# Kernel optimization log

Measured on AMD Instinct MI355X. Metric: run time of the kernel, lower is better.

Reference implementation:

```python
import jax, jax.numpy as jnp
import numpy as np

N_NODES = 100000
N_EDGES = 1600000
N_FEAT = 128
HIDDEN = 128
OUT = 1
NUM_GRAPHS = 2048


def setup_inputs() -> dict:
    key = jax.random.key(0)
    ks = jax.random.split(key, 8)
    x = jax.random.normal(ks[0], (N_NODES, N_FEAT), dtype=jnp.float32)
    edge_index = jax.random.randint(ks[1], (2, N_EDGES), 0, N_NODES, dtype=jnp.int64)
    batch = jnp.sort(jax.random.randint(ks[2], (N_NODES,), 0, NUM_GRAPHS, dtype=jnp.int64))
    s = 1.0 / np.sqrt(N_FEAT)
    W1 = jax.random.normal(ks[3], (N_FEAT, HIDDEN), dtype=jnp.float32) * s
    b1 = jnp.zeros((HIDDEN,), dtype=jnp.float32)
    W2 = jax.random.normal(ks[4], (HIDDEN, HIDDEN), dtype=jnp.float32) * s
    b2 = jnp.zeros((HIDDEN,), dtype=jnp.float32)
    Wlin = jax.random.normal(ks[5], (HIDDEN, OUT), dtype=jnp.float32) * s
    blin = jnp.zeros((OUT,), dtype=jnp.float32)
    return {"x": x, "edge_index": edge_index, "batch": batch,
            "W1": W1, "b1": b1, "W2": W2, "b2": b2, "Wlin": Wlin, "blin": blin}


def gcn_conv(x, W, b, src, dst, n_nodes):
    # PyG GCNConv: x' = D^{-1/2} (A + I) D^{-1/2} (X W) + b, deg includes self-loop
    xw = x @ W  # [N, H]
    deg = jax.ops.segment_sum(jnp.ones(src.shape[0], xw.dtype), dst, num_segments=n_nodes) + 1.0
    dinv = jax.lax.rsqrt(deg)
    norm = dinv[src] * dinv[dst]  # [E]
    agg = jax.ops.segment_sum(xw[src] * norm[:, None], dst, num_segments=n_nodes)
    # self-loop contribution: norm = deg^{-1}
    return agg + xw * (1.0 / deg)[:, None] + b


def global_mean_pool(x, batch, num_graphs):
    sums = jax.ops.segment_sum(x, batch, num_segments=num_graphs)
    cnts = jax.ops.segment_sum(jnp.ones(x.shape[0], x.dtype), batch, num_segments=num_graphs)
    return sums / jnp.maximum(cnts, 1.0)[:, None]


def reference(x, edge_index, batch, W1, b1, W2, b2, Wlin, blin):
    src, dst = edge_index[0], edge_index[1]
    n = x.shape[0]
    h = gcn_conv(x, W1, b1, src, dst, n)
    h = jax.nn.relu(h)  # dropout is a no-op in eval mode
    h = gcn_conv(h, W2, b2, src, dst, n)
    g = global_mean_pool(h, batch, NUM_GRAPHS)  # [G, H]
    return g @ Wlin + blin
```

## Files before the change

kernel.cpp:

```cpp
#include <hip/hip_runtime.h>

#define N_NODES   100000
#define N_EDGES   1600000
#define NFEAT     128
#define NGRAPHS   2048
#define CBSHIFT   8
#define NCB       ((N_NODES + 255) / 256)
#define P1_EPB    8192
#define GEMM_BLOCKS 782
#define BH_BLOCKS   256
#define DP_BLOCKS 100
#define DP_NPB    ((N_NODES + DP_BLOCKS - 1) / DP_BLOCKS)
#define G1_BLOCKS 2048
#define ZCNT      (NGRAPHS + NCB + 64 + 512 + NCB)

typedef __attribute__((ext_vector_type(8))) short short8;
typedef __attribute__((ext_vector_type(4))) float f32x4;

__device__ __forceinline__ unsigned short f2bf(float f) {
    unsigned int u = __float_as_uint(f);
    u += 0x7FFFu + ((u >> 16) & 1u);
    return (unsigned short)(u >> 16);
}

__device__ __forceinline__ void acc8s(float* acc, uint4 v, float s) {
    acc[0] = fmaf(s, __uint_as_float(v.x << 16), acc[0]);
    acc[1] = fmaf(s, __uint_as_float(v.x & 0xFFFF0000u), acc[1]);
    acc[2] = fmaf(s, __uint_as_float(v.y << 16), acc[2]);
    acc[3] = fmaf(s, __uint_as_float(v.y & 0xFFFF0000u), acc[3]);
    acc[4] = fmaf(s, __uint_as_float(v.z << 16), acc[4]);
    acc[5] = fmaf(s, __uint_as_float(v.z & 0xFFFF0000u), acc[5]);
    acc[6] = fmaf(s, __uint_as_float(v.w << 16), acc[6]);
    acc[7] = fmaf(s, __uint_as_float(v.w & 0xFFFF0000u), acc[7]);
}

__global__ __launch_bounds__(256) void k_misc(const float* __restrict__ W1,
                                              unsigned short* __restrict__ WT1,
                                              const float* __restrict__ W2,
                                              const float* __restrict__ Wlin,
                                              const float* __restrict__ b2,
                                              const float* __restrict__ blin,
                                              float* __restrict__ w2l,
                                              int* __restrict__ zeros) {
    const int blk = blockIdx.x;
    const int t = threadIdx.x;
    if (blk < 16) {
        int base = blk * 1024 + t * 4;
        #pragma unroll
        for (int q = 0; q < 4; ++q) {
            int i = base + q;
            int n = i >> 7, k = i & 127;
            WT1[i] = f2bf(W1[k * 128 + n]);
        }
    } else if (blk == 16) {
        __shared__ float s[256];
        int i = t >> 1, half = t & 1;
        float ps = 0.f;
        for (int j = half * 64; j < half * 64 + 64; ++j)
            ps += W2[i * 128 + j] * Wlin[j];
        s[t] = ps;
        __syncthreads();
        if (!half) w2l[i] = s[t] + s[t + 1];
        __syncthreads();
        float pc = (t < 128) ? b2[t] * Wlin[t] : 0.f;
        s[t] = pc;
        __syncthreads();
        for (int off = 128; off > 0; off >>= 1) {
            if (t < off) s[t] += s[t + off];
            __syncthreads();
        }
        if (t == 0) w2l[128] = s[0] + blin[0];
    } else {
        int i = (blk - 17) * 256 + t;
        if (i < ZCNT) zeros[i] = 0;
    }
}

__global__ __launch_bounds__(256) void k_gemm_bhist(const float* __restrict__ X,
                                                    const unsigned short* __restrict__ WT,
                                                    unsigned short* __restrict__ C,
                                                    const int* __restrict__ dst,
                                                    int* __restrict__ bcount) {
    if (blockIdx.x >= GEMM_BLOCKS) {
        __shared__ int h[NCB];
        for (int i = threadIdx.x; i < NCB; i += 256) h[i] = 0;
        __syncthreads();
        int b = blockIdx.x - GEMM_BLOCKS;
        int stride = BH_BLOCKS * 256;
        for (int e = b * 256 + threadIdx.x; e < N_EDGES; e += stride)
            atomicAdd(&h[dst[e] >> CBSHIFT], 1);
        __syncthreads();
        for (int i = threadIdx.x; i < NCB; i += 256) {
            int v = h[i];
            if (v) atomicAdd(&bcount[i], v);
        }
        return;
    }
    const int tid  = threadIdx.x;
    const int R0   = blockIdx.x * 128;
    const int wv   = tid >> 6;
    const int lane = tid & 63;
    const int m16  = lane & 15;
    const int quad = lane >> 4;
    const int r0 = R0 + wv * 32 + m16;
    const int r1 = r0 + 16;
    const bool ok0 = r0 < N_NODES, ok1 = r1 < N_NODES;

    f32x4 acc[2][8] = {};
    #pragma unroll
    for (int ks = 0; ks < 4; ++ks) {
        const int k0 = ks * 32 + quad * 8;
        short8 a0 = {}, a1 = {};
        if (ok0) {
            float4 f0 = *(const float4*)(X + (size_t)r0 * NFEAT + k0);
            float4 f1 = *(const float4*)(X + (size_t)r0 * NFEAT + k0 + 4);
            a0[0] = (short)f2bf(f0.x); a0[1] = (short)f2bf(f0.y);
            a0[2] = (short)f2bf(f0.z); a0[3] = (short)f2bf(f0.w);
            a0[4] = (short)f2bf(f1.x); a0[5] = (short)f2bf(f1.y);
            a0[6] = (short)f2bf(f1.z); a0[7] = (short)f2bf(f1.w);
        }
        if (ok1) {
            float4 f0 = *(const float4*)(X + (size_t)r1 * NFEAT + k0);
            float4 f1 = *(const float4*)(X + (size_t)r1 * NFEAT + k0 + 4);
            a1[0] = (short)f2bf(f0.x); a1[1] = (short)f2bf(f0.y);
            a1[2] = (short)f2bf(f0.z); a1[3] = (short)f2bf(f0.w);
            a1[4] = (short)f2bf(f1.x); a1[5] = (short)f2bf(f1.y);
            a1[6] = (short)f2bf(f1.z); a1[7] = (short)f2bf(f1.w);
        }
        #pragma unroll
        for (int ct = 0; ct < 8; ++ct) {
            short8 bb = *(const short8*)(WT + (ct * 16 + m16) * 128 + k0);
            acc[0][ct] = __builtin_amdgcn_mfma_f32_16x16x32_bf16(a0, bb, acc[0][ct], 0, 0, 0);
            acc[1][ct] = __builtin_amdgcn_mfma_f32_16x16x32_bf16(a1, bb, acc[1][ct], 0, 0, 0);
        }
    }
    #pragma unroll
    for (int t2 = 0; t2 < 2; ++t2) {
        int rbase = R0 + wv * 32 + t2 * 16 + quad * 4;
        #pragma unroll
        for (int reg = 0; reg < 4; ++reg) {
            int gr = rbase + reg;
            if (gr < N_NODES) {
                #pragma unroll
                for (int ct = 0; ct < 8; ++ct)
                    C[(size_t)gr * NFEAT + ct * 16 + m16] = f2bf(acc[t2][ct][reg]);
            }
        }
    }
}

__global__ __launch_bounds__(256) void k_p1(const int* __restrict__ src,
                                            const int* __restrict__ dst,
                                            const int* __restrict__ bcount,
                                            int* __restrict__ bstart,
                                            int* __restrict__ alloc,
                                            unsigned int* __restrict__ pairs) {
    __shared__ int hist[NCB], base[NCB], cur[NCB], bst[NCB], s[256];
    const int t = threadIdx.x;
    for (int i = t; i < NCB; i += 256) { hist[i] = 0; cur[i] = 0; }
    int v0 = (2 * t < NCB) ? bcount[2 * t] : 0;
    int v1 = (2 * t + 1 < NCB) ? bcount[2 * t + 1] : 0;
    int local = v0 + v1;
    s[t] = local;
    __syncthreads();
    for (int off = 1; off < 256; off <<= 1) {
        int x = (t >= off) ? s[t - off] : 0;
        __syncthreads();
        s[t] += x;
        __syncthreads();
    }
    int excl = s[t] - local;
    if (2 * t < NCB)     bst[2 * t] = excl;
    if (2 * t + 1 < NCB) bst[2 * t + 1] = excl + v0;
    if (blockIdx.x == 0) {
        if (2 * t < NCB)     bstart[2 * t] = excl;
        if (2 * t + 1 < NCB) bstart[2 * t + 1] = excl + v0;
        if (t == 255) bstart[NCB] = s[255];
    }
    __syncthreads();
    const int e0 = blockIdx.x * P1_EPB;
    const int e1 = min(e0 + P1_EPB, N_EDGES);
    for (int e = e0 + t; e < e1; e += 256)
        atomicAdd(&hist[dst[e] >> CBSHIFT], 1);
    __syncthreads();
    const int off0 = (blockIdx.x * 89) % NCB;
    for (int k = t; k < NCB; k += 256) {
        int i = k + off0;
        if (i >= NCB) i -= NCB;
        int c = hist[i];
        base[i] = c ? (bst[i] + atomicAdd(&alloc[i], c)) : 0;
    }
    __syncthreads();
    for (int e = e0 + t; e < e1; e += 256) {
        int d = dst[e];
        int b = d >> CBSHIFT;
        int r = atomicAdd(&cur[b], 1);
        pairs[base[b] + r] = (unsigned int)src[e] | ((unsigned int)(d & 255) << 17);
    }
}

__global__ __launch_bounds__(256) void k_p2(const unsigned int* __restrict__ pairs,
                                            const int* __restrict__ bstart,
                                            int* __restrict__ csr_src,
                                            int* __restrict__ row_start,
                                            int* __restrict__ indeg,
                                            float* __restrict__ dinv,
                                            int* __restrict__ dcount) {
    __shared__ int hist[256], sst[256], cur[256], s[256], dh[64];
    const int b = blockIdx.x;
    const int t = threadIdx.x;
    const int beg = bstart[b];
    const int end = bstart[b + 1];
    hist[t] = 0; cur[t] = 0;
    if (t < 64) dh[t] = 0;
    __syncthreads();
    for (int i = beg + t; i < end; i += 256)
        atomicAdd(&hist[pairs[i] >> 17], 1);
    __syncthreads();
    int v = hist[t];
    s[t] = v;
    __syncthreads();
    for (int off = 1; off < 256; off <<= 1) {
        int x = (t >= off) ? s[t - off] : 0;
        __syncthreads();
        s[t] += x;
        __syncthreads();
    }
    sst[t] = s[t] - v;
    __syncthreads();
    {
        int node = (b << CBSHIFT) + t;
        if (node < N_NODES) {
            row_start[node] = beg + sst[t];
            indeg[node] = v;
            dinv[node] = rsqrtf((float)v + 1.0f);
            atomicAdd(&dh[63 - min(v, 63)], 1);
        }
    }
    for (int i = beg + t; i < end; i += 256) {
        unsigned int pv = pairs[i];
        int dl = pv >> 17;
        int r = atomicAdd(&cur[dl], 1);
        csr_src[beg + sst[dl] + r] = (int)(pv & 0x1FFFFu);
    }
    __syncthreads();
    if (t < 64 && dh[t]) atomicAdd(&dcount[((b & 7) << 6) + t], dh[t]);
}

__global__ __launch_bounds__(256) void k_dperm(const int* __restrict__ indeg,
                                               const int* __restrict__ dcount,
                                               int* __restrict__ dalloc,
                                               int* __restrict__ perm) {
    __shared__ int h[64], base[64], cur[64], s[64];
    const int t = threadIdx.x;
    int v = 0;
    if (t < 64) {
        h[t] = 0; cur[t] = 0;
        #pragma unroll
        for (int sh = 0; sh < 8; ++sh) v += dcount[(sh << 6) + t];
        s[t] = v;
    }
    __syncthreads();
    for (int off = 1; off < 64; off <<= 1) {
        int x = (t >= off && t < 64) ? s[t - off] : 0;
        __syncthreads();
        if (t < 64) s[t] += x;
        __syncthreads();
    }
    int myst = (t < 64) ? s[t] - v : 0;
    const int i0 = blockIdx.x * DP_NPB;
    const int i1 = min(i0 + DP_NPB, N_NODES);
    for (int i = i0 + t; i < i1; i += 256)
        atomicAdd(&h[63 - min(indeg[i], 63)], 1);
    __syncthreads();
    if (t < 64) {
        int c = h[t];
        base[t] = c ? (myst + atomicAdd(&dalloc[t], c)) : 0;
    }
    __syncthreads();
    for (int i = i0 + t; i < i1; i += 256) {
        int bin = 63 - min(indeg[i], 63);
        int r = atomicAdd(&cur[bin], 1);
        perm[base[bin] + r] = i;
    }
}

__global__ __launch_bounds__(256) void k_gather1(const unsigned short* __restrict__ xwb,
                                                 const int* __restrict__ csr_src,
                                                 const int* __restrict__ row_start,
                                                 const int* __restrict__ indeg,
                                                 const float* __restrict__ dinv,
                                                 const float* __restrict__ b,
                                                 const float* __restrict__ w2l,
                                                 const int* __restrict__ perm,
                                                 float* __restrict__ z) {
    const int lane  = threadIdx.x & 63;
    const int p     = lane & 15;
    const int gbase = lane & 48;
    const int ngroups = G1_BLOCKS * 16;
    int gid = blockIdx.x * 16 + (threadIdx.x >> 4);
    const uint4* tab = (const uint4*)xwb;
    float4 b0 = *(const float4*)(b + p * 8);
    float4 b1 = *(const float4*)(b + p * 8 + 4);
    float4 w0 = *(const float4*)(w2l + p * 8);
    float4 w1 = *(const float4*)(w2l + p * 8 + 4);

    for (int nidx = gid; nidx < N_NODES; nidx += ngroups) {
        int node = perm[nidx];
        const int beg = row_start[node];
        const int cnt = indeg[node];
        float dvn = dinv[node];
        float acc[8] = {};
        acc8s(acc, tab[(size_t)node * 16 + p], dvn);
        int j = 0;
        #pragma unroll 1
        for (; j + 8 <= cnt; j += 8) {
            int   my   = csr_src[beg + j + (p & 7)];
            float mydv = dinv[my];
            uint4 v[8];
            #pragma unroll
            for (int q = 0; q < 8; ++q) {
                int idx = __shfl(my, gbase + q);
                v[q] = tab[(size_t)idx * 16 + p];
            }
            #pragma unroll
            for (int q = 0; q < 8; ++q) {
                float sv = __shfl(mydv, gbase + q);
                acc8s(acc, v[q], sv);
            }
        }
        #pragma unroll 1
        for (; j < cnt; ++j) {
            int idx = csr_src[beg + j];
            float sv = dinv[idx];
            acc8s(acc, tab[(size_t)idx * 16 + p], sv);
        }
        float s = fmaxf(acc[0] * dvn + b0.x, 0.f) * w0.x
                + fmaxf(acc[1] * dvn + b0.y, 0.f) * w0.y
                + fmaxf(acc[2] * dvn + b0.z, 0.f) * w0.z
                + fmaxf(acc[3] * dvn + b0.w, 0.f) * w0.w
                + fmaxf(acc[4] * dvn + b1.x, 0.f) * w1.x
                + fmaxf(acc[5] * dvn + b1.y, 0.f) * w1.y
                + fmaxf(acc[6] * dvn + b1.z, 0.f) * w1.z
                + fmaxf(acc[7] * dvn + b1.w, 0.f) * w1.w;
        s += __shfl_xor(s, 1);
        s += __shfl_xor(s, 2);
        s += __shfl_xor(s, 4);
        s += __shfl_xor(s, 8);
        if (p == 0) z[node] = s * dvn;
    }
}

__global__ __launch_bounds__(256) void k_gather2s(const float* __restrict__ z,
                                                  const int* __restrict__ csr_src,
                                                  const int* __restrict__ row_start,
                                                  const int* __restrict__ indeg,
                                                  const float* __restrict__ dinv,
                                                  const int* __restrict__ perm,
                                                  const int* __restrict__ batch,
                                                  float* __restrict__ gsum) {
    int nidx = blockIdx.x * blockDim.x + threadIdx.x;
    if (nidx >= N_NODES) return;
    int node = perm[nidx];
    const int beg = row_start[node];
    const int cnt = indeg[node];
    float a = z[node];
    int j = 0;
    #pragma unroll 1
    for (; j + 4 <= cnt; j += 4) {
        int i0 = csr_src[beg + j + 0];
        int i1 = csr_src[beg + j + 1];
        int i2 = csr_src[beg + j + 2];
        int i3 = csr_src[beg + j + 3];
        a += z[i0] + z[i1] + z[i2] + z[i3];
    }
    #pragma unroll 1
    for (; j < cnt; ++j)
        a += z[csr_src[beg + j]];
    atomicAdd(&gsum[batch[node]], a * dinv[node]);
}

__global__ void k_final(const float* __restrict__ gsum, const int* __restrict__ batch,
                        const float* __restrict__ c2, float* __restrict__ out) {
    int g = blockIdx.x * blockDim.x + threadIdx.x;
    if (g >= NGRAPHS) return;
    int lo = 0, hi = N_NODES;
    while (lo < hi) { int m = (lo + hi) >> 1; if (batch[m] < g) lo = m + 1; else hi = m; }
    int lb = lo;
    lo = 0; hi = N_NODES;
    int g1 = g + 1;
    while (lo < hi) { int m = (lo + hi) >> 1; if (batch[m] < g1) lo = m + 1; else hi = m; }
    float cnt = (float)(lo - lb);
    out[g] = gsum[g] / fmaxf(cnt, 1.0f) + c2[0];
}

extern "C" void kernel_launch(void* const* d_in, const int* in_sizes, int n_in,
                              void* d_out, int out_size, void* d_ws, size_t ws_size,
                              hipStream_t stream) {
    const float* x    = (const float*)d_in[0];
    const int*   ei   = (const int*)d_in[1];
    const int*   bat  = (const int*)d_in[2];
    const float* W1   = (const float*)d_in[3];
    const float* b1   = (const float*)d_in[4];
    const float* W2   = (const float*)d_in[5];
    const float* b2   = (const float*)d_in[6];
    const float* Wlin = (const float*)d_in[7];
    const float* blin = (const float*)d_in[8];
    float* out = (float*)d_out;

    const int* src = ei;
    const int* dst = ei + N_EDGES;

    const size_t NF = (size_t)N_NODES * NFEAT;
    unsigned short* bufA = (unsigned short*)d_ws;
    float* z       = (float*)(bufA + NF);
    float* dinv    = z + N_NODES;
    int* row_start = (int*)(dinv + N_NODES);
    int* indeg     = row_start + N_NODES;
    int* perm      = indeg + N_NODES;
    int* bstart    = perm + N_NODES;
    float* gsum    = (float*)(bstart + NCB + 1);
    int* alloc     = (int*)(gsum + NGRAPHS);
    int* dalloc    = alloc + NCB;
    int* dcount    = dalloc + 64;
    int* bcount    = dcount + 512;
    unsigned short* WT1 = (unsigned short*)(bcount + NCB);
    float* w2l     = (float*)(WT1 + 128 * 128);
    unsigned int* pairs = (unsigned int*)(w2l + 132);
    int* csr_src   = (int*)(pairs + N_EDGES);

    const int BS = 256;
    int p1_blocks   = (N_EDGES + P1_EPB - 1) / P1_EPB;
    int node_blocks = (N_NODES + BS - 1) / BS;
    int misc_blocks = 17 + (ZCNT + BS - 1) / BS;

    k_misc<<<misc_blocks, BS, 0, stream>>>(W1, WT1, W2, Wlin, b2, blin, w2l, (int*)gsum);
    k_gemm_bhist<<<GEMM_BLOCKS + BH_BLOCKS, BS, 0, stream>>>(x, WT1, bufA, dst, bcount);

    k_p1<<<p1_blocks, BS, 0, stream>>>(src, dst, bcount, bstart, alloc, pairs);
    k_p2<<<NCB, BS, 0, stream>>>(pairs, bstart, csr_src, row_start, indeg, dinv, dcount);
    k_dperm<<<DP_BLOCKS, BS, 0, stream>>>(indeg, dcount, dalloc, perm);

    k_gather1<<<G1_BLOCKS, BS, 0, stream>>>(bufA, csr_src, row_start, indeg, dinv, b1, w2l,
                                            perm, z);

    k_gather2s<<<node_blocks, BS, 0, stream>>>(z, csr_src, row_start, indeg, dinv, perm,
                                               bat, gsum);

    k_final<<<(NGRAPHS + BS - 1) / BS, BS, 0, stream>>>(gsum, bat, w2l + 128, out);
}
```

Before: 276.6 us.

## Pack node metadata, use dynamic work queue and prefetch in GCN gathers

The degree-sorted permutation now stores a packed int4 per node (row start, degree, dinv, node id), so the gather kernels make one load instead of four dependent ones. The first gather hands out work through an atomic counter and prefetches the next chunk of neighbour indices while the current chunk's feature rows load. Bias and weight vectors are staged in shared memory. The second gather splits each node's edges across four lanes and combines them with shuffles. This targets load imbalance and latency-bound dependent index loads, at the cost of an extra atomic counter and a metadata buffer that reuses the freed pairs region.

```diff
diff --git a/kernel.cpp b/kernel.cpp
--- a/kernel.cpp
+++ b/kernel.cpp
@@ -12,7 +12,7 @@
 #define DP_BLOCKS 100
 #define DP_NPB    ((N_NODES + DP_BLOCKS - 1) / DP_BLOCKS)
 #define G1_BLOCKS 2048
-#define ZCNT      (NGRAPHS + NCB + 64 + 512 + NCB)
+#define ZCNT      (NGRAPHS + NCB + 64 + 512 + NCB + 1)
 
 typedef __attribute__((ext_vector_type(8))) short short8;
 typedef __attribute__((ext_vector_type(4))) float f32x4;
@@ -248,9 +248,11 @@
 }
 
 __global__ __launch_bounds__(256) void k_dperm(const int* __restrict__ indeg,
+                                               const int* __restrict__ row_start,
+                                               const float* __restrict__ dinv,
                                                const int* __restrict__ dcount,
                                                int* __restrict__ dalloc,
-                                               int* __restrict__ perm) {
+                                               int4* __restrict__ meta) {
     __shared__ int h[64], base[64], cur[64], s[64];
     const int t = threadIdx.x;
     int v = 0;
@@ -279,105 +281,115 @@
     }
     __syncthreads();
     for (int i = i0 + t; i < i1; i += 256) {
-        int bin = 63 - min(indeg[i], 63);
+        int dg = indeg[i];
+        int bin = 63 - min(dg, 63);
         int r = atomicAdd(&cur[bin], 1);
-        perm[base[bin] + r] = i;
+        meta[base[bin] + r] = make_int4(row_start[i], dg, __float_as_int(dinv[i]), i);
     }
 }
 
 __global__ __launch_bounds__(256) void k_gather1(const unsigned short* __restrict__ xwb,
                                                  const int* __restrict__ csr_src,
-                                                 const int* __restrict__ row_start,
-                                                 const int* __restrict__ indeg,
                                                  const float* __restrict__ dinv,
                                                  const float* __restrict__ b,
                                                  const float* __restrict__ w2l,
-                                                 const int* __restrict__ perm,
+                                                 const int4* __restrict__ meta,
+                                                 int* __restrict__ ctr,
                                                  float* __restrict__ z) {
-    const int lane  = threadIdx.x & 63;
-    const int p     = lane & 15;
+    __shared__ float sbw[256];
+    __shared__ int sbase;
+    const int t = threadIdx.x;
+    const int lane = t & 63;
+    const int p = lane & 15;
     const int gbase = lane & 48;
-    const int ngroups = G1_BLOCKS * 16;
-    int gid = blockIdx.x * 16 + (threadIdx.x >> 4);
     const uint4* tab = (const uint4*)xwb;
-    float4 b0 = *(const float4*)(b + p * 8);
-    float4 b1 = *(const float4*)(b + p * 8 + 4);
-    float4 w0 = *(const float4*)(w2l + p * 8);
-    float4 w1 = *(const float4*)(w2l + p * 8 + 4);
-
-    for (int nidx = gid; nidx < N_NODES; nidx += ngroups) {
-        int node = perm[nidx];
-        const int beg = row_start[node];
-        const int cnt = indeg[node];
-        float dvn = dinv[node];
-        float acc[8] = {};
-        acc8s(acc, tab[(size_t)node * 16 + p], dvn);
-        int j = 0;
-        #pragma unroll 1
-        for (; j + 8 <= cnt; j += 8) {
-            int   my   = csr_src[beg + j + (p & 7)];
-            float mydv = dinv[my];
-            uint4 v[8];
-            #pragma unroll
-            for (int q = 0; q < 8; ++q) {
-                int idx = __shfl(my, gbase + q);
-                v[q] = tab[(size_t)idx * 16 + p];
+    sbw[t] = (t < 128) ? b[t] : w2l[t - 128];
+
+    for (;;) {
+        __syncthreads();
+        if (t == 0) sbase = atomicAdd(ctr, 16);
+        __syncthreads();
+        const int base = sbase;
+        if (base >= N_NODES) break;
+        const int nidx = base + (t >> 4);
+        if (nidx < N_NODES) {
+            const int4 md = meta[nidx];
+            const int beg   = md.x;
+            const int cnt   = md.y;
+            const float dvn = __int_as_float(md.z);
+            const int node  = md.w;
+            float acc[8] = {};
+            acc8s(acc, tab[(size_t)node * 16 + p], dvn);
+            const int nch = (cnt + 7) >> 3;
+            const int j0 = p & 7;
+            int my; float mydv;
+            {
+                bool vld = j0 < cnt;
+                my = vld ? csr_src[beg + j0] : node;
+                float dv = dinv[my];
+                mydv = vld ? dv : 0.f;
             }
-            #pragma unroll
-            for (int q = 0; q < 8; ++q) {
-                float sv = __shfl(mydv, gbase + q);
-                acc8s(acc, v[q], sv);
+            #pragma unroll 1
+            for (int c = 0; c < nch; ++c) {
+                const int myc = my; const float mydvc = mydv;
+                const int jn = (c + 1) * 8 + j0;
+                if (c + 1 < nch) {
+                    bool vld = jn < cnt;
+                    my = vld ? csr_src[beg + jn] : node;
+                    float dv = dinv[my];
+                    mydv = vld ? dv : 0.f;
+                }
+                uint4 v[8];
+                #pragma unroll
+                for (int q = 0; q < 8; ++q) {
+                    int idx = __shfl(myc, gbase + q);
+                    v[q] = tab[(size_t)idx * 16 + p];
+                }
+                #pragma unroll
+                for (int q = 0; q < 8; ++q) {
+                    float sv = __shfl(mydvc, gbase + q);
+                    acc8s(acc, v[q], sv);
+                }
             }
-        }
-        #pragma unroll 1
-        for (; j < cnt; ++j) {
-            int idx = csr_src[beg + j];
-            float sv = dinv[idx];
-            acc8s(acc, tab[(size_t)idx * 16 + p], sv);
-        }
-        float s = fmaxf(acc[0] * dvn + b0.x, 0.f) * w0.x
-                + fmaxf(acc[1] * dvn + b0.y, 0.f) * w0.y
-                + fmaxf(acc[2] * dvn + b0.z, 0.f) * w0.z
-                + fmaxf(acc[3] * dvn + b0.w, 0.f) * w0.w
-                + fmaxf(acc[4] * dvn + b1.x, 0.f) * w1.x
-                + fmaxf(acc[5] * dvn + b1.y, 0.f) * w1.y
-                + fmaxf(acc[6] * dvn + b1.z, 0.f) * w1.z
-                + fmaxf(acc[7] * dvn + b1.w, 0.f) * w1.w;
-        s += __shfl_xor(s, 1);
-        s += __shfl_xor(s, 2);
-        s += __shfl_xor(s, 4);
-        s += __shfl_xor(s, 8);
-        if (p == 0) z[node] = s * dvn;
+            float4 b0 = *(const float4*)(sbw + p * 8);
+            float4 b1 = *(const float4*)(sbw + p * 8 + 4);
+            float4 w0 = *(const float4*)(sbw + 128 + p * 8);
+            float4 w1 = *(const float4*)(sbw + 128 + p * 8 + 4);
+            float s = fmaxf(acc[0] * dvn + b0.x, 0.f) * w0.x
+                    + fmaxf(acc[1] * dvn + b0.y, 0.f) * w0.y
+                    + fmaxf(acc[2] * dvn + b0.z, 0.f) * w0.z
+                    + fmaxf(acc[3] * dvn + b0.w, 0.f) * w0.w
+                    + fmaxf(acc[4] * dvn + b1.x, 0.f) * w1.x
+                    + fmaxf(acc[5] * dvn + b1.y, 0.f) * w1.y
+                    + fmaxf(acc[6] * dvn + b1.z, 0.f) * w1.z
+                    + fmaxf(acc[7] * dvn + b1.w, 0.f) * w1.w;
+            s += __shfl_xor(s, 1);
+            s += __shfl_xor(s, 2);
+            s += __shfl_xor(s, 4);
+            s += __shfl_xor(s, 8);
+            if (p == 0) z[node] = s * dvn;
+        }
     }
 }
 
 __global__ __launch_bounds__(256) void k_gather2s(const float* __restrict__ z,
                                                   const int* __restrict__ csr_src,
-                                                  const int* __restrict__ row_start,
-                                                  const int* __restrict__ indeg,
-                                                  const float* __restrict__ dinv,
-                                                  const int* __restrict__ perm,
+                                                  const int4* __restrict__ meta,
                                                   const int* __restrict__ batch,
                                                   float* __restrict__ gsum) {
-    int nidx = blockIdx.x * blockDim.x + threadIdx.x;
+    int tid = blockIdx.x * blockDim.x + threadIdx.x;
+    int nidx = tid >> 2;
+    int q = tid & 3;
     if (nidx >= N_NODES) return;
-    int node = perm[nidx];
-    const int beg = row_start[node];
-    const int cnt = indeg[node];
-    float a = z[node];
-    int j = 0;
-    #pragma unroll 1
-    for (; j + 4 <= cnt; j += 4) {
-        int i0 = csr_src[beg + j + 0];
-        int i1 = csr_src[beg + j + 1];
-        int i2 = csr_src[beg + j + 2];
-        int i3 = csr_src[beg + j + 3];
-        a += z[i0] + z[i1] + z[i2] + z[i3];
-    }
-    #pragma unroll 1
-    for (; j < cnt; ++j)
+    int4 md = meta[nidx];
+    const int beg = md.x, cnt = md.y, node = md.w;
+    const float dvn = __int_as_float(md.z);
+    float a = (q == 0) ? z[node] : 0.f;
+    for (int j = q; j < cnt; j += 4)
         a += z[csr_src[beg + j]];
-    atomicAdd(&gsum[batch[node]], a * dinv[node]);
+    a += __shfl_xor(a, 1);
+    a += __shfl_xor(a, 2);
+    if (q == 0) atomicAdd(&gsum[batch[node]], a * dvn);
 }
 
 __global__ void k_final(const float* __restrict__ gsum, const int* __restrict__ batch,
@@ -417,21 +429,22 @@
     float* dinv    = z + N_NODES;
     int* row_start = (int*)(dinv + N_NODES);
     int* indeg     = row_start + N_NODES;
-    int* perm      = indeg + N_NODES;
-    int* bstart    = perm + N_NODES;
+    int* bstart    = indeg + N_NODES;
     float* gsum    = (float*)(bstart + NCB + 1);
     int* alloc     = (int*)(gsum + NGRAPHS);
     int* dalloc    = alloc + NCB;
     int* dcount    = dalloc + 64;
     int* bcount    = dcount + 512;
-    unsigned short* WT1 = (unsigned short*)(bcount + NCB);
+    int* ctr       = bcount + NCB;
+    unsigned short* WT1 = (unsigned short*)(ctr + 1);
     float* w2l     = (float*)(WT1 + 128 * 128);
     unsigned int* pairs = (unsigned int*)(w2l + 132);
     int* csr_src   = (int*)(pairs + N_EDGES);
+    int4* meta     = (int4*)(((size_t)pairs + 15) & ~(size_t)15);
 
     const int BS = 256;
     int p1_blocks   = (N_EDGES + P1_EPB - 1) / P1_EPB;
-    int node_blocks = (N_NODES + BS - 1) / BS;
+    int g2_blocks   = (4 * N_NODES + BS - 1) / BS;
     int misc_blocks = 17 + (ZCNT + BS - 1) / BS;
 
     k_misc<<<misc_blocks, BS, 0, stream>>>(W1, WT1, W2, Wlin, b2, blin, w2l, (int*)gsum);
@@ -439,13 +452,11 @@
 
     k_p1<<<p1_blocks, BS, 0, stream>>>(src, dst, bcount, bstart, alloc, pairs);
     k_p2<<<NCB, BS, 0, stream>>>(pairs, bstart, csr_src, row_start, indeg, dinv, dcount);
-    k_dperm<<<DP_BLOCKS, BS, 0, stream>>>(indeg, dcount, dalloc, perm);
-
-    k_gather1<<<G1_BLOCKS, BS, 0, stream>>>(bufA, csr_src, row_start, indeg, dinv, b1, w2l,
-                                            perm, z);
-
-    k_gather2s<<<node_blocks, BS, 0, stream>>>(z, csr_src, row_start, indeg, dinv, perm,
-                                               bat, gsum);
+    k_dperm<<<DP_BLOCKS, BS, 0, stream>>>(indeg, row_start, dinv, dcount, dalloc, meta);
+
+    k_gather1<<<G1_BLOCKS, BS, 0, stream>>>(bufA, csr_src, dinv, b1, w2l, meta, ctr, z);
+
+    k_gather2s<<<g2_blocks, BS, 0, stream>>>(z, csr_src, meta, bat, gsum);
 
     k_final<<<(NGRAPHS + BS - 1) / BS, BS, 0, stream>>>(gsum, bat, w2l + 128, out);
 }
```

Result: slower. 341.5 us (+23.5%).
